# Kernel optimization log

Measured on AMD Instinct MI355X. Metric: run time of the kernel, lower is better.

Reference implementation:

```python
import jax, jax.numpy as jnp
import numpy as np

B, T, D_IN = 1024, 512, 32   # batch, sequence_length, input_dim
H = 512                      # hidden_dim
P = 96                       # prediction_length
D_OUT = 1                    # output_dim


def setup_inputs() -> dict:
    key = jax.random.key(0)
    ks = jax.random.split(key, 24)
    s = 1.0 / np.sqrt(H)  # PyTorch GRU default init scale
    u = lambda k, shape: jax.random.uniform(k, shape, jnp.float32, -s, s)
    inp = {"x": jax.random.normal(ks[0], (B, T, D_IN), jnp.float32)}
    # Encoder GRU: layer0 input D_IN, layer1 input H. Gate order: r, z, n.
    inp["enc_Wih0"] = u(ks[1], (3 * H, D_IN)); inp["enc_Whh0"] = u(ks[2], (3 * H, H))
    inp["enc_bih0"] = u(ks[3], (3 * H,));      inp["enc_bhh0"] = u(ks[4], (3 * H,))
    inp["enc_Wih1"] = u(ks[5], (3 * H, H));    inp["enc_Whh1"] = u(ks[6], (3 * H, H))
    inp["enc_bih1"] = u(ks[7], (3 * H,));      inp["enc_bhh1"] = u(ks[8], (3 * H,))
    # Decoder GRU: layer0 input D_OUT, layer1 input H.
    inp["dec_Wih0"] = u(ks[9], (3 * H, D_OUT)); inp["dec_Whh0"] = u(ks[10], (3 * H, H))
    inp["dec_bih0"] = u(ks[11], (3 * H,));      inp["dec_bhh0"] = u(ks[12], (3 * H,))
    inp["dec_Wih1"] = u(ks[13], (3 * H, H));    inp["dec_Whh1"] = u(ks[14], (3 * H, H))
    inp["dec_bih1"] = u(ks[15], (3 * H,));      inp["dec_bhh1"] = u(ks[16], (3 * H,))
    # Output projection + learned decoder start token.
    inp["out_W"] = u(ks[17], (D_OUT, H)); inp["out_b"] = u(ks[18], (D_OUT,))
    inp["dec_start"] = jnp.zeros((1, 1, D_OUT), jnp.float32)
    return inp


def gru_cell(x, h, Wih, Whh, bih, bhh):
    # PyTorch GRU cell: r,z,n gate order.
    gi = x @ Wih.T + bih          # [B, 3H]
    gh = h @ Whh.T + bhh          # [B, 3H]
    ir, iz, inn = jnp.split(gi, 3, axis=-1)
    hr, hz, hn = jnp.split(gh, 3, axis=-1)
    r = jax.nn.sigmoid(ir + hr)
    z = jax.nn.sigmoid(iz + hz)
    n = jnp.tanh(inn + r * hn)
    return (1.0 - z) * n + z * h


def reference(x,
              enc_Wih0, enc_Whh0, enc_bih0, enc_bhh0,
              enc_Wih1, enc_Whh1, enc_bih1, enc_bhh1,
              dec_Wih0, dec_Whh0, dec_bih0, dec_bhh0,
              dec_Wih1, dec_Whh1, dec_bih1, dec_bhh1,
              out_W, out_b, dec_start):
    Bsz = x.shape[0]
    h0 = jnp.zeros((Bsz, H), x.dtype)

    def enc_step(carry, xt):
        h1, h2 = carry
        h1 = gru_cell(xt, h1, enc_Wih0, enc_Whh0, enc_bih0, enc_bhh0)
        h2 = gru_cell(h1, h2, enc_Wih1, enc_Whh1, enc_bih1, enc_bhh1)
        return (h1, h2), None

    (h1, h2), _ = jax.lax.scan(enc_step, (h0, h0), jnp.swapaxes(x, 0, 1))

    y0 = jnp.broadcast_to(dec_start[0], (Bsz, D_OUT)).astype(x.dtype)

    def dec_step(carry, _):
        d1, d2, y = carry
        d1 = gru_cell(y, d1, dec_Wih0, dec_Whh0, dec_bih0, dec_bhh0)
        d2 = gru_cell(d1, d2, dec_Wih1, dec_Whh1, dec_bih1, dec_bhh1)
        y = d2 @ out_W.T + out_b  # [B, D_OUT]
        return (d1, d2, y), y

    _, ys = jax.lax.scan(dec_step, (h1, h2, y0), None, length=P)
    return jnp.swapaxes(ys, 0, 1)  # [B, P, D_OUT]
```

## Files before the change

kernel.cpp:

```cpp
#include <hip/hip_runtime.h>

#define HD 512
#define BB 1024
#define TT 512
#define PP 96
#define DIN 32
#define KC_H 16
#define NBLK 256
#define GRPB 16

typedef unsigned short u16;
typedef __attribute__((ext_vector_type(8))) short bf16x8;
typedef __attribute__((ext_vector_type(4))) float f32x4;
typedef __attribute__((address_space(3))) unsigned int lds_u32;
typedef __attribute__((address_space(3))) u16 lds_u16;
typedef __attribute__((address_space(1))) unsigned int glb_u32;

#define WAIT_VM(N) asm volatile("s_waitcnt vmcnt(" #N ")" ::: "memory")
__device__ __forceinline__ void bar_raw() { asm volatile("s_barrier" ::: "memory"); }

__device__ __forceinline__ float bf2f(u16 s) {
  return __uint_as_float(((unsigned)s) << 16);
}
__device__ __forceinline__ u16 f2bf_rne(float f) {
  unsigned u = __float_as_uint(f);
  u += 0x7FFF + ((u >> 16) & 1);
  return (u16)(u >> 16);
}
__device__ __forceinline__ float sigm(float v) { return 1.f / (1.f + __expf(-v)); }
__device__ __forceinline__ float tanh_(float a) {
  return 1.f - 2.f / (__expf(2.f * a) + 1.f);
}

__device__ __forceinline__ bf16x8 load_sc16(const u16* p) {
  bf16x8 r;
  asm volatile("global_load_dwordx4 %0, %1, off sc0 sc1" : "=&v"(r) : "v"(p) : "memory");
  return r;
}
__device__ __forceinline__ void store_sc_u16(u16* p, unsigned v) {
  asm volatile("global_store_short %0, %1, off sc0 sc1" :: "v"(p), "v"(v) : "memory");
}
__device__ __forceinline__ void store_sc_f32(float* p, float v) {
  asm volatile("global_store_dword %0, %1, off sc0 sc1" :: "v"(p), "v"(v) : "memory");
}
__device__ __forceinline__ float load_sc_f32w(const float* p) {
  float v;
  asm volatile("global_load_dword %0, %1, off sc0 sc1\ns_waitcnt vmcnt(0)"
               : "=&v"(v) : "v"(p) : "memory");
  return v;
}
__device__ __forceinline__ unsigned load_sc_u32w(const unsigned* p) {
  unsigned v;
  asm volatile("global_load_dword %0, %1, off sc0 sc1\ns_waitcnt vmcnt(0)"
               : "=&v"(v) : "v"(p) : "memory");
  return v;
}
__device__ __forceinline__ void store_h_sc(u16* H, u16* L, size_t idx, float hv) {
  u16 hi = (u16)(__float_as_uint(hv) >> 16);
  u16 lo = f2bf_rne(hv - bf2f(hi));
  store_sc_u16(H + idx, (unsigned)hi);
  store_sc_u16(L + idx, (unsigned)lo);
}

__global__ void pack_w_kernel(const float* __restrict__ W, int K,
                              u16* __restrict__ out) {
  int tid = blockIdx.x * 256 + threadIdx.x;
  int KC = K >> 5;
  int total = 16 * KC * 2 * 6 * 64;
  if (tid >= total) return;
  int lane = tid & 63;
  int rest = tid >> 6;
  int gs = rest % 6; rest /= 6;
  int fc = rest & 1; rest >>= 1;
  int kc = rest % KC;
  int jb = rest / KC;
  int g = gs >> 1, s = gs & 1;
  int j = jb * 32 + fc * 16 + (lane & 15);
  int k = kc * 32 + (lane >> 4) * 8;
  const float* src = W + (size_t)(g * HD + j) * K + k;
  bf16x8 v;
#pragma unroll
  for (int i = 0; i < 8; ++i) {
    float f = src[i];
    u16 hi = f2bf_rne(f);
    v[i] = (short)((s == 0) ? hi : f2bf_rne(f - bf2f(hi)));
  }
  *(bf16x8*)(out + (size_t)tid * 8) = v;
}

struct AF { bf16x8 h[2]; bf16x8 l[2]; };

__device__ __forceinline__ void fence_af(AF& a) {
  asm volatile("" : "+v"(a.h[0]), "+v"(a.h[1]), "+v"(a.l[0]), "+v"(a.l[1]));
}
__device__ __forceinline__ void load_af_sc(AF& a, const u16* aH0, const u16* aL0, int kc) {
  const u16* p = aH0 + kc * 32;
  const u16* q = aL0 + kc * 32;
  a.h[0] = load_sc16(p);
  a.h[1] = load_sc16(p + 16 * HD);
  a.l[0] = load_sc16(q);
  a.l[1] = load_sc16(q + 16 * HD);
}

__device__ __forceinline__ void mfma_kc_l(const lds_u16* base, int lane,
                                          const AF& a, f32x4* aR, f32x4* aZ, f32x4* aN) {
  typedef __attribute__((address_space(3))) const bf16x8 lds_bf16x8;
  const lds_u16* p = base + lane * 8;
#pragma unroll
  for (int g = 0; g < 3; ++g) {
    f32x4* acc = (g == 0) ? aR : (g == 1) ? aZ : aN;
    bf16x8 whi = *(lds_bf16x8*)(p + (g * 2 + 0) * 512);
    bf16x8 wlo = *(lds_bf16x8*)(p + (g * 2 + 1) * 512);
#pragma unroll
    for (int s = 0; s < 2; ++s) {
      acc[s] = __builtin_amdgcn_mfma_f32_16x16x32_bf16(a.h[s], whi, acc[s], 0, 0, 0);
      acc[s] = __builtin_amdgcn_mfma_f32_16x16x32_bf16(a.l[s], whi, acc[s], 0, 0, 0);
      acc[s] = __builtin_amdgcn_mfma_f32_16x16x32_bf16(a.h[s], wlo, acc[s], 0, 0, 0);
    }
  }
}
__device__ __forceinline__ void mfma_kc_g(const u16* base, int lane,
                                          const AF& a, f32x4* aR, f32x4* aZ, f32x4* aN) {
  const u16* p = base + lane * 8;
#pragma unroll
  for (int g = 0; g < 3; ++g) {
    f32x4* acc = (g == 0) ? aR : (g == 1) ? aZ : aN;
    bf16x8 whi = *(const bf16x8*)(p + (g * 2 + 0) * 512);
    bf16x8 wlo = *(const bf16x8*)(p + (g * 2 + 1) * 512);
#pragma unroll
    for (int s = 0; s < 2; ++s) {
      acc[s] = __builtin_amdgcn_mfma_f32_16x16x32_bf16(a.h[s], whi, acc[s], 0, 0, 0);
      acc[s] = __builtin_amdgcn_mfma_f32_16x16x32_bf16(a.l[s], whi, acc[s], 0, 0, 0);
      acc[s] = __builtin_amdgcn_mfma_f32_16x16x32_bf16(a.h[s], wlo, acc[s], 0, 0, 0);
    }
  }
}

__device__ __forceinline__ void stage6(const u16* src, u16* dst, int lane) {
#pragma unroll
  for (int j = 0; j < 6; ++j)
    __builtin_amdgcn_global_load_lds((const glb_u32*)(src + j * 512 + lane * 8),
                                     (lds_u32*)(dst + j * 512), 16, 0, 0);
}

template <bool DUAL>
__device__ __forceinline__ void pipe_phase(
    u16* ringfc, const u16* Ahi, const u16* Alo,
    const u16* WA, const u16* WB, int row0w, int lane, bool stg,
    f32x4* aR, f32x4* aZ, f32x4* aN,
    f32x4* bR, f32x4* bZ, f32x4* bN) {
  const int quad = lane >> 4, n16 = lane & 15;
  const u16* aH0 = Ahi + (size_t)(row0w + n16) * HD + quad * 8;
  const u16* aL0 = Alo + (size_t)(row0w + n16) * HD + quad * 8;
  u16* pb[4] = {ringfc, ringfc + 6144, ringfc + 2 * 6144, ringfc + 3 * 6144};
  AF a0, a1, a2, a3;

  auto issueB = [&](int ikc, u16* pair, AF& dst) {
    if (stg) {
      stage6(WA + (size_t)ikc * 6144, pair, lane);
      if constexpr (DUAL) stage6(WB + (size_t)ikc * 6144, pair + 3072, lane);
    }
    load_af_sc(dst, aH0, aL0, ikc);
  };
  auto cons = [&](u16* pair, AF& a) {
    fence_af(a);
    mfma_kc_l((const lds_u16*)pair, lane, a, aR, aZ, aN);
    if constexpr (DUAL) mfma_kc_l((const lds_u16*)(pair + 3072), lane, a, bR, bZ, bN);
  };
  auto wsteady = [&]() {
    if (stg) { if constexpr (DUAL) WAIT_VM(32); else WAIT_VM(20); }
    else WAIT_VM(8);
  };
  auto wtail1 = [&]() {
    if (stg) { if constexpr (DUAL) WAIT_VM(16); else WAIT_VM(10); }
    else WAIT_VM(4);
  };

  WAIT_VM(0);
  issueB(0, pb[0], a0);
  issueB(1, pb[1], a1);
  issueB(2, pb[2], a2);
#pragma unroll 1
  for (int kc = 0; kc < 12; kc += 4) {
    wsteady(); bar_raw(); issueB(kc + 3, pb[3], a3); cons(pb[0], a0);
    wsteady(); bar_raw(); issueB(kc + 4, pb[0], a0); cons(pb[1], a1);
    wsteady(); bar_raw(); issueB(kc + 5, pb[1], a1); cons(pb[2], a2);
    wsteady(); bar_raw(); issueB(kc + 6, pb[2], a2); cons(pb[3], a3);
  }
  wsteady(); bar_raw(); issueB(15, pb[3], a3); cons(pb[0], a0);
  wsteady(); bar_raw(); cons(pb[1], a1);
  wtail1();  bar_raw(); cons(pb[2], a2);
  WAIT_VM(0); bar_raw(); cons(pb[3], a3);
}

__device__ __forceinline__ void x_phase(const float* x, int t, const u16* Wp,
                                        int jb, int fc, int row0w, int lane,
                                        f32x4* aR, f32x4* aZ, f32x4* aN) {
  const int quad = lane >> 4, n16 = lane & 15;
  AF ax;
#pragma unroll
  for (int s = 0; s < 2; ++s) {
    const float* xp = x + (size_t)(row0w + s * 16 + n16) * (TT * DIN) +
                      (size_t)t * DIN + quad * 8;
    f32x4 v0 = *(const f32x4*)xp;
    f32x4 v1 = *(const f32x4*)(xp + 4);
    bf16x8 hi, lo;
#pragma unroll
    for (int i = 0; i < 8; ++i) {
      float f = (i < 4) ? v0[i] : v1[i - 4];
      u16 h = (u16)(__float_as_uint(f) >> 16);
      hi[i] = (short)h;
      lo[i] = (short)f2bf_rne(f - bf2f(h));
    }
    ax.h[s] = hi;
    ax.l[s] = lo;
  }
  mfma_kc_g(Wp + ((size_t)jb * 2 + fc) * 3072, lane, ax, aR, aZ, aN);
}

__device__ __forceinline__ void gbar(unsigned* gen, unsigned target) {
  WAIT_VM(0);
  __syncthreads();
  if (threadIdx.x == 0) {
    atomicAdd(gen, 1u);
    while (load_sc_u32w(gen) < target) __builtin_amdgcn_s_sleep(2);
  }
  __syncthreads();
}

__device__ __forceinline__ void gru_epi_reg(
    const float* bi, const float* bh, float (*ht)[4],
    u16* hnH, u16* hnL, int col, int row0w, int quad,
    const f32x4* aR, const f32x4* aZ, const f32x4* aNX, const f32x4* aNH) {
  const float bir = bi[col],          bhr = bh[col];
  const float biz = bi[HD + col],     bhz = bh[HD + col];
  const float bin = bi[2 * HD + col], bhn = bh[2 * HD + col];
#pragma unroll
  for (int s = 0; s < 2; ++s)
#pragma unroll
    for (int r = 0; r < 4; ++r) {
      const int row = row0w + s * 16 + quad * 4 + r;
      const size_t idx = (size_t)row * HD + col;
      float rr = sigm(aR[s][r] + bir + bhr);
      float zz = sigm(aZ[s][r] + biz + bhz);
      float nn = tanh_(aNX[s][r] + bin + rr * (aNH[s][r] + bhn));
      float hv = (1.f - zz) * nn + zz * ht[s][r];
      ht[s][r] = hv;
      store_h_sc(hnH, hnL, idx, hv);
    }
}

__global__ __launch_bounds__(256, 1)
void gru_persistent_kernel(
    const float* x,
    const u16* pkX0, const u16* pkH0, const float* bi0, const float* bh0,
    const u16* pkX1, const u16* pkH1, const float* bi1, const float* bh1,
    const u16* pkD0H, const float* dbi0, const float* dbh0, const float* dW0,
    const u16* pkD1I, const u16* pkD1H, const float* dbi1, const float* dbh1,
    const float* outW, const float* outb, const float* dstart,
    u16* h1aH, u16* h1aL, u16* h1bH, u16* h1bL,
    u16* h2aH, u16* h2aL, u16* h2bH, u16* h2bL,
    float* yfull, float* dout, unsigned* gen) {
  __shared__ u16 ring[2][4][6144];
  const int b = blockIdx.x;
  const int jb = (b & 7) * 2 + ((b >> 3) & 1);
  const int row0 = (b >> 4) * 64;
  const int tid = threadIdx.x, wave = tid >> 6, lane = tid & 63;
  const int quad = lane >> 4, n16 = lane & 15;
  const int fc = wave & 1, rowg = wave >> 1;
  const bool stg = (rowg == 0);
  const int row0w = row0 + rowg * 32;
  const int col = jb * 32 + fc * 16 + n16;
  u16* ringfc = &ring[fc][0][0];
  const f32x4 z4 = {0.f, 0.f, 0.f, 0.f};
  const size_t woff = ((size_t)jb * KC_H * 2 + fc) * 3072;
  unsigned* geng = gen + ((b >> 4) << 6);

  u16 *h1cH = h1aH, *h1cL = h1aL, *h1nH = h1bH, *h1nL = h1bL;
  u16 *h2cH = h2aH, *h2cL = h2aL, *h2nH = h2bH, *h2nL = h2bL;
  float ht1[2][4] = {{0, 0, 0, 0}, {0, 0, 0, 0}};
  float ht2[2][4] = {{0, 0, 0, 0}, {0, 0, 0, 0}};
  unsigned it = 0;

  for (int k = 0; k <= TT; ++k) {
    f32x4 R0[2] = {z4, z4}, Z0[2] = {z4, z4}, NX0[2] = {z4, z4}, NH0[2] = {z4, z4};
    f32x4 R1[2] = {z4, z4}, Z1[2] = {z4, z4}, NX1[2] = {z4, z4}, NH1[2] = {z4, z4};
    if (k > 0 && k < TT) {
      pipe_phase<true>(ringfc, h1cH, h1cL, pkH0 + woff, pkX1 + woff,
                       row0w, lane, stg, R0, Z0, NH0, R1, Z1, NX1);
    } else if (k == 0) {
      pipe_phase<false>(ringfc, h1cH, h1cL, pkH0 + woff, pkH0 + woff,
                        row0w, lane, stg, R0, Z0, NH0, R1, Z1, NX1);
    } else {
      pipe_phase<false>(ringfc, h1cH, h1cL, pkX1 + woff, pkX1 + woff,
                        row0w, lane, stg, R1, Z1, NX1, R0, Z0, NH0);
    }
    if (k < TT) {
      x_phase(x, k, pkX0, jb, fc, row0w, lane, R0, Z0, NX0);
      gru_epi_reg(bi0, bh0, ht1, h1nH, h1nL, col, row0w, quad, R0, Z0, NX0, NH0);
    }
    if (k > 0) {
      pipe_phase<false>(ringfc, h2cH, h2cL, pkH1 + woff, pkH1 + woff,
                        row0w, lane, stg, R1, Z1, NH1, R0, Z0, NX0);
      gru_epi_reg(bi1, bh1, ht2, h2nH, h2nL, col, row0w, quad, R1, Z1, NX1, NH1);
    }
    gbar(geng, GRPB * (++it));
    if (k < TT) { u16* t0 = h1cH; h1cH = h1nH; h1nH = t0;
                  u16* t1 = h1cL; h1cL = h1nL; h1nL = t1; }
    if (k > 0)  { u16* t0 = h2cH; h2cH = h2nH; h2nH = t0;
                  u16* t1 = h2cL; h2cL = h2nL; h2nL = t1; }
  }

  for (int t = 0; t < PP; ++t) {
    {
      f32x4 R[2] = {z4, z4}, Z[2] = {z4, z4}, NH[2] = {z4, z4};
      f32x4 D0[2] = {z4, z4}, D1[2] = {z4, z4}, D2[2] = {z4, z4};
      pipe_phase<false>(ringfc, h1cH, h1cL, pkD0H + woff, pkD0H + woff,
                        row0w, lane, stg, R, Z, NH, D0, D1, D2);
      float yl[2][4] = {{0, 0, 0, 0}, {0, 0, 0, 0}};
      if (t > 0) {
        const float* yb = yfull + ((t - 1) & 1) * BB;
#pragma unroll
        for (int s = 0; s < 2; ++s)
#pragma unroll
          for (int r = 0; r < 4; ++r) {
            const float* p = yb + (row0w + s * 16 + quad * 4 + r);
            asm volatile("global_load_dword %0, %1, off sc0 sc1"
                         : "=&v"(yl[s][r]) : "v"(p) : "memory");
          }
        WAIT_VM(0);
#pragma unroll
        for (int s = 0; s < 2; ++s)
#pragma unroll
          for (int r = 0; r < 4; ++r)
            asm volatile("" : "+v"(yl[s][r]));
      }
      const float ds0 = dstart[0], ob0 = outb[0];
      const float bir = dbi0[col],          bhr = dbh0[col];
      const float biz = dbi0[HD + col],     bhz = dbh0[HD + col];
      const float bin = dbi0[2 * HD + col], bhn = dbh0[2 * HD + col];
      const float w0r = dW0[col], w0z = dW0[HD + col], w0n = dW0[2 * HD + col];
#pragma unroll
      for (int s = 0; s < 2; ++s)
#pragma unroll
        for (int r = 0; r < 4; ++r) {
          const int row = row0w + s * 16 + quad * 4 + r;
          const size_t idx = (size_t)row * HD + col;
          float yv = (t == 0) ? ds0 : (ob0 + yl[s][r]);
          if (t > 0 && jb == 0 && fc == 0 && n16 == 0)
            dout[(size_t)row * PP + (t - 1)] = yv;
          float rr = sigm(R[s][r] + bir + bhr + yv * w0r);
          float zz = sigm(Z[s][r] + biz + bhz + yv * w0z);
          float nn = tanh_(bin + yv * w0n + rr * (NH[s][r] + bhn));
          float hv = (1.f - zz) * nn + zz * ht1[s][r];
          ht1[s][r] = hv;
          store_h_sc(h1nH, h1nL, idx, hv);
        }
    }
    gbar(geng, GRPB * (++it));
    {
      f32x4 R[2] = {z4, z4}, Z[2] = {z4, z4}, NX[2] = {z4, z4}, NH[2] = {z4, z4};
      f32x4 D0[2] = {z4, z4}, D1[2] = {z4, z4}, D2[2] = {z4, z4};
      pipe_phase<false>(ringfc, h1nH, h1nL, pkD1I + woff, pkD1I + woff,
                        row0w, lane, stg, R, Z, NX, D0, D1, D2);
      pipe_phase<false>(ringfc, h2cH, h2cL, pkD1H + woff, pkD1H + woff,
                        row0w, lane, stg, R, Z, NH, D0, D1, D2);
      const float bir = dbi1[col],          bhr = dbh1[col];
      const float biz = dbi1[HD + col],     bhz = dbh1[HD + col];
      const float bin = dbi1[2 * HD + col], bhn = dbh1[2 * HD + col];
      const float wo = outW[col];
      float* yw = yfull + (t & 1) * BB;
      float* yz = yfull + ((t - 1) & 1) * BB;
#pragma unroll
      for (int s = 0; s < 2; ++s)
#pragma unroll
        for (int r = 0; r < 4; ++r) {
          const int row = row0w + s * 16 + quad * 4 + r;
          const size_t idx = (size_t)row * HD + col;
          float rr = sigm(R[s][r] + bir + bhr);
          float zz = sigm(Z[s][r] + biz + bhz);
          float nn = tanh_(NX[s][r] + bin + rr * (NH[s][r] + bhn));
          float hv = (1.f - zz) * nn + zz * ht2[s][r];
          ht2[s][r] = hv;
          store_h_sc(h2nH, h2nL, idx, hv);
          float v = hv * wo;
#pragma unroll
          for (int off = 1; off < 16; off <<= 1) v += __shfl_xor(v, off, 16);
          if (n16 == 0) {
            atomicAdd(yw + row, v);
            if (t > 0 && jb == 0 && fc == 0) store_sc_f32(yz + row, 0.f);
          }
        }
    }
    gbar(geng, GRPB * (++it));
    { u16* t0 = h1cH; h1cH = h1nH; h1nH = t0;
      u16* t1 = h1cL; h1cL = h1nL; h1nL = t1; }
    { u16* t0 = h2cH; h2cH = h2nH; h2nH = t0;
      u16* t1 = h2cL; h2cL = h2nL; h2nL = t1; }
  }

  if ((b & 15) == 0 && tid < 64) {
    int row = row0 + tid;
    float v = load_sc_f32w(yfull + ((PP - 1) & 1) * BB + row);
    dout[(size_t)row * PP + (PP - 1)] = outb[0] + v;
  }
}

extern "C" void kernel_launch(void* const* d_in, const int* in_sizes, int n_in,
                              void* d_out, int out_size, void* d_ws, size_t ws_size,
                              hipStream_t stream) {
  const float* x      = (const float*)d_in[0];
  const float* eW_ih0 = (const float*)d_in[1];
  const float* eW_hh0 = (const float*)d_in[2];
  const float* eb_ih0 = (const float*)d_in[3];
  const float* eb_hh0 = (const float*)d_in[4];
  const float* eW_ih1 = (const float*)d_in[5];
  const float* eW_hh1 = (const float*)d_in[6];
  const float* eb_ih1 = (const float*)d_in[7];
  const float* eb_hh1 = (const float*)d_in[8];
  const float* dW_ih0 = (const float*)d_in[9];
  const float* dW_hh0 = (const float*)d_in[10];
  const float* db_ih0 = (const float*)d_in[11];
  const float* db_hh0 = (const float*)d_in[12];
  const float* dW_ih1 = (const float*)d_in[13];
  const float* dW_hh1 = (const float*)d_in[14];
  const float* db_ih1 = (const float*)d_in[15];
  const float* db_hh1 = (const float*)d_in[16];
  const float* outW   = (const float*)d_in[17];
  const float* outb   = (const float*)d_in[18];
  const float* dstart = (const float*)d_in[19];
  float* out = (float*)d_out;

  char* w = (char*)d_ws;
  size_t off = 0;
  auto carve = [&](size_t bytes) -> void* {
    void* p = w + off;
    off = (off + bytes + 255) & ~(size_t)255;
    return p;
  };
  u16* h1aH = (u16*)carve((size_t)BB * HD * 2); u16* h1aL = (u16*)carve((size_t)BB * HD * 2);
  u16* h1bH = (u16*)carve((size_t)BB * HD * 2); u16* h1bL = (u16*)carve((size_t)BB * HD * 2);
  u16* h2aH = (u16*)carve((size_t)BB * HD * 2); u16* h2aL = (u16*)carve((size_t)BB * HD * 2);
  u16* h2bH = (u16*)carve((size_t)BB * HD * 2); u16* h2bL = (u16*)carve((size_t)BB * HD * 2);
  float* yfull = (float*)carve((size_t)2 * BB * 4);
  unsigned* gen = (unsigned*)carve(4096);
  auto carve_pack = [&](int K) -> u16* {
    return (u16*)carve((size_t)3 * HD * K * 2 * 2);
  };
  u16* pk_e0ih = carve_pack(DIN);
  u16* pk_e0hh = carve_pack(HD);
  u16* pk_e1ih = carve_pack(HD);
  u16* pk_e1hh = carve_pack(HD);
  u16* pk_d0hh = carve_pack(HD);
  u16* pk_d1ih = carve_pack(HD);
  u16* pk_d1hh = carve_pack(HD);

  hipMemsetAsync(h1aH, 0, (size_t)BB * HD * 2, stream);
  hipMemsetAsync(h1aL, 0, (size_t)BB * HD * 2, stream);
  hipMemsetAsync(h2aH, 0, (size_t)BB * HD * 2, stream);
  hipMemsetAsync(h2aL, 0, (size_t)BB * HD * 2, stream);
  hipMemsetAsync(yfull, 0, (size_t)2 * BB * 4, stream);
  hipMemsetAsync(gen, 0, 4096, stream);

  auto pack = [&](const float* W, int K, u16* dst) {
    int total = 16 * (K >> 5) * 2 * 6 * 64;
    pack_w_kernel<<<(total + 255) / 256, 256, 0, stream>>>(W, K, dst);
  };
  pack(eW_ih0, DIN, pk_e0ih);
  pack(eW_hh0, HD, pk_e0hh);
  pack(eW_ih1, HD, pk_e1ih);
  pack(eW_hh1, HD, pk_e1hh);
  pack(dW_hh0, HD, pk_d0hh);
  pack(dW_ih1, HD, pk_d1ih);
  pack(dW_hh1, HD, pk_d1hh);

  gru_persistent_kernel<<<NBLK, 256, 0, stream>>>(
      x, pk_e0ih, pk_e0hh, eb_ih0, eb_hh0,
      pk_e1ih, pk_e1hh, eb_ih1, eb_hh1,
      pk_d0hh, db_ih0, db_hh0, dW_ih0,
      pk_d1ih, pk_d1hh, db_ih1, db_hh1,
      outW, outb, dstart,
      h1aH, h1aL, h1bH, h1bL, h2aH, h2aL, h2bH, h2bL,
      yfull, out, gen);
}
```

Measured before the change: 17.02 ms.

## Double waves per block, each wave handling 16 rows instead of 32

Each block now launches 512 threads instead of 256. Every wave computes one 16-row MFMA tile instead of two, which halves per-wave accumulator and A-fragment registers and doubles the number of waves per block. The vmcnt wait thresholds are reduced to match the smaller number of loads per stage. The aim is more latency hiding across waves, at the cost of more waves contending for the shared LDS ring and the barriers. launch_bounds is changed to (512, 2).

```diff
diff --git a/kernel.cpp b/kernel.cpp
--- a/kernel.cpp
+++ b/kernel.cpp
@@ -88,51 +88,41 @@
   *(bf16x8*)(out + (size_t)tid * 8) = v;
 }
 
-struct AF { bf16x8 h[2]; bf16x8 l[2]; };
+struct AF { bf16x8 h; bf16x8 l; };
 
 __device__ __forceinline__ void fence_af(AF& a) {
-  asm volatile("" : "+v"(a.h[0]), "+v"(a.h[1]), "+v"(a.l[0]), "+v"(a.l[1]));
+  asm volatile("" : "+v"(a.h), "+v"(a.l));
 }
 __device__ __forceinline__ void load_af_sc(AF& a, const u16* aH0, const u16* aL0, int kc) {
-  const u16* p = aH0 + kc * 32;
-  const u16* q = aL0 + kc * 32;
-  a.h[0] = load_sc16(p);
-  a.h[1] = load_sc16(p + 16 * HD);
-  a.l[0] = load_sc16(q);
-  a.l[1] = load_sc16(q + 16 * HD);
-}
-
-__device__ __forceinline__ void mfma_kc_l(const lds_u16* base, int lane,
-                                          const AF& a, f32x4* aR, f32x4* aZ, f32x4* aN) {
+  a.h = load_sc16(aH0 + kc * 32);
+  a.l = load_sc16(aL0 + kc * 32);
+}
+
+__device__ __forceinline__ void mfma_kc_l(const lds_u16* base, int lane, const AF& a,
+                                          f32x4& aR, f32x4& aZ, f32x4& aN) {
   typedef __attribute__((address_space(3))) const bf16x8 lds_bf16x8;
   const lds_u16* p = base + lane * 8;
 #pragma unroll
   for (int g = 0; g < 3; ++g) {
-    f32x4* acc = (g == 0) ? aR : (g == 1) ? aZ : aN;
+    f32x4* acc = (g == 0) ? &aR : (g == 1) ? &aZ : &aN;
     bf16x8 whi = *(lds_bf16x8*)(p + (g * 2 + 0) * 512);
     bf16x8 wlo = *(lds_bf16x8*)(p + (g * 2 + 1) * 512);
-#pragma unroll
-    for (int s = 0; s < 2; ++s) {
-      acc[s] = __builtin_amdgcn_mfma_f32_16x16x32_bf16(a.h[s], whi, acc[s], 0, 0, 0);
-      acc[s] = __builtin_amdgcn_mfma_f32_16x16x32_bf16(a.l[s], whi, acc[s], 0, 0, 0);
-      acc[s] = __builtin_amdgcn_mfma_f32_16x16x32_bf16(a.h[s], wlo, acc[s], 0, 0, 0);
-    }
-  }
-}
-__device__ __forceinline__ void mfma_kc_g(const u16* base, int lane,
-                                          const AF& a, f32x4* aR, f32x4* aZ, f32x4* aN) {
+    *acc = __builtin_amdgcn_mfma_f32_16x16x32_bf16(a.h, whi, *acc, 0, 0, 0);
+    *acc = __builtin_amdgcn_mfma_f32_16x16x32_bf16(a.l, whi, *acc, 0, 0, 0);
+    *acc = __builtin_amdgcn_mfma_f32_16x16x32_bf16(a.h, wlo, *acc, 0, 0, 0);
+  }
+}
+__device__ __forceinline__ void mfma_kc_g(const u16* base, int lane, const AF& a,
+                                          f32x4& aR, f32x4& aZ, f32x4& aN) {
   const u16* p = base + lane * 8;
 #pragma unroll
   for (int g = 0; g < 3; ++g) {
-    f32x4* acc = (g == 0) ? aR : (g == 1) ? aZ : aN;
+    f32x4* acc = (g == 0) ? &aR : (g == 1) ? &aZ : &aN;
     bf16x8 whi = *(const bf16x8*)(p + (g * 2 + 0) * 512);
     bf16x8 wlo = *(const bf16x8*)(p + (g * 2 + 1) * 512);
-#pragma unroll
-    for (int s = 0; s < 2; ++s) {
-      acc[s] = __builtin_amdgcn_mfma_f32_16x16x32_bf16(a.h[s], whi, acc[s], 0, 0, 0);
-      acc[s] = __builtin_amdgcn_mfma_f32_16x16x32_bf16(a.l[s], whi, acc[s], 0, 0, 0);
-      acc[s] = __builtin_amdgcn_mfma_f32_16x16x32_bf16(a.h[s], wlo, acc[s], 0, 0, 0);
-    }
+    *acc = __builtin_amdgcn_mfma_f32_16x16x32_bf16(a.h, whi, *acc, 0, 0, 0);
+    *acc = __builtin_amdgcn_mfma_f32_16x16x32_bf16(a.l, whi, *acc, 0, 0, 0);
+    *acc = __builtin_amdgcn_mfma_f32_16x16x32_bf16(a.h, wlo, *acc, 0, 0, 0);
   }
 }
 
@@ -147,8 +137,8 @@
 __device__ __forceinline__ void pipe_phase(
     u16* ringfc, const u16* Ahi, const u16* Alo,
     const u16* WA, const u16* WB, int row0w, int lane, bool stg,
-    f32x4* aR, f32x4* aZ, f32x4* aN,
-    f32x4* bR, f32x4* bZ, f32x4* bN) {
+    f32x4& aR, f32x4& aZ, f32x4& aN,
+    f32x4& bR, f32x4& bZ, f32x4& bN) {
   const int quad = lane >> 4, n16 = lane & 15;
   const u16* aH0 = Ahi + (size_t)(row0w + n16) * HD + quad * 8;
   const u16* aL0 = Alo + (size_t)(row0w + n16) * HD + quad * 8;
@@ -168,12 +158,12 @@
     if constexpr (DUAL) mfma_kc_l((const lds_u16*)(pair + 3072), lane, a, bR, bZ, bN);
   };
   auto wsteady = [&]() {
-    if (stg) { if constexpr (DUAL) WAIT_VM(32); else WAIT_VM(20); }
-    else WAIT_VM(8);
+    if (stg) { if constexpr (DUAL) WAIT_VM(28); else WAIT_VM(16); }
+    else WAIT_VM(4);
   };
   auto wtail1 = [&]() {
-    if (stg) { if constexpr (DUAL) WAIT_VM(16); else WAIT_VM(10); }
-    else WAIT_VM(4);
+    if (stg) { if constexpr (DUAL) WAIT_VM(14); else WAIT_VM(8); }
+    else WAIT_VM(2);
   };
 
   WAIT_VM(0);
@@ -195,26 +185,23 @@
 
 __device__ __forceinline__ void x_phase(const float* x, int t, const u16* Wp,
                                         int jb, int fc, int row0w, int lane,
-                                        f32x4* aR, f32x4* aZ, f32x4* aN) {
+                                        f32x4& aR, f32x4& aZ, f32x4& aN) {
   const int quad = lane >> 4, n16 = lane & 15;
   AF ax;
-#pragma unroll
-  for (int s = 0; s < 2; ++s) {
-    const float* xp = x + (size_t)(row0w + s * 16 + n16) * (TT * DIN) +
-                      (size_t)t * DIN + quad * 8;
-    f32x4 v0 = *(const f32x4*)xp;
-    f32x4 v1 = *(const f32x4*)(xp + 4);
-    bf16x8 hi, lo;
-#pragma unroll
-    for (int i = 0; i < 8; ++i) {
-      float f = (i < 4) ? v0[i] : v1[i - 4];
-      u16 h = (u16)(__float_as_uint(f) >> 16);
-      hi[i] = (short)h;
-      lo[i] = (short)f2bf_rne(f - bf2f(h));
-    }
-    ax.h[s] = hi;
-    ax.l[s] = lo;
-  }
+  const float* xp = x + (size_t)(row0w + n16) * (TT * DIN) +
+                    (size_t)t * DIN + quad * 8;
+  f32x4 v0 = *(const f32x4*)xp;
+  f32x4 v1 = *(const f32x4*)(xp + 4);
+  bf16x8 hi, lo;
+#pragma unroll
+  for (int i = 0; i < 8; ++i) {
+    float f = (i < 4) ? v0[i] : v1[i - 4];
+    u16 h = (u16)(__float_as_uint(f) >> 16);
+    hi[i] = (short)h;
+    lo[i] = (short)f2bf_rne(f - bf2f(h));
+  }
+  ax.h = hi;
+  ax.l = lo;
   mfma_kc_g(Wp + ((size_t)jb * 2 + fc) * 3072, lane, ax, aR, aZ, aN);
 }
 
@@ -229,28 +216,26 @@
 }
 
 __device__ __forceinline__ void gru_epi_reg(
-    const float* bi, const float* bh, float (*ht)[4],
+    const float* bi, const float* bh, float* ht,
     u16* hnH, u16* hnL, int col, int row0w, int quad,
-    const f32x4* aR, const f32x4* aZ, const f32x4* aNX, const f32x4* aNH) {
+    const f32x4& aR, const f32x4& aZ, const f32x4& aNX, const f32x4& aNH) {
   const float bir = bi[col],          bhr = bh[col];
   const float biz = bi[HD + col],     bhz = bh[HD + col];
   const float bin = bi[2 * HD + col], bhn = bh[2 * HD + col];
 #pragma unroll
-  for (int s = 0; s < 2; ++s)
-#pragma unroll
-    for (int r = 0; r < 4; ++r) {
-      const int row = row0w + s * 16 + quad * 4 + r;
-      const size_t idx = (size_t)row * HD + col;
-      float rr = sigm(aR[s][r] + bir + bhr);
-      float zz = sigm(aZ[s][r] + biz + bhz);
-      float nn = tanh_(aNX[s][r] + bin + rr * (aNH[s][r] + bhn));
-      float hv = (1.f - zz) * nn + zz * ht[s][r];
-      ht[s][r] = hv;
-      store_h_sc(hnH, hnL, idx, hv);
-    }
-}
-
-__global__ __launch_bounds__(256, 1)
+  for (int r = 0; r < 4; ++r) {
+    const int row = row0w + quad * 4 + r;
+    const size_t idx = (size_t)row * HD + col;
+    float rr = sigm(aR[r] + bir + bhr);
+    float zz = sigm(aZ[r] + biz + bhz);
+    float nn = tanh_(aNX[r] + bin + rr * (aNH[r] + bhn));
+    float hv = (1.f - zz) * nn + zz * ht[r];
+    ht[r] = hv;
+    store_h_sc(hnH, hnL, idx, hv);
+  }
+}
+
+__global__ __launch_bounds__(512, 2)
 void gru_persistent_kernel(
     const float* x,
     const u16* pkX0, const u16* pkH0, const float* bi0, const float* bh0,
@@ -269,7 +254,7 @@
   const int quad = lane >> 4, n16 = lane & 15;
   const int fc = wave & 1, rowg = wave >> 1;
   const bool stg = (rowg == 0);
-  const int row0w = row0 + rowg * 32;
+  const int row0w = row0 + rowg * 16;
   const int col = jb * 32 + fc * 16 + n16;
   u16* ringfc = &ring[fc][0][0];
   const f32x4 z4 = {0.f, 0.f, 0.f, 0.f};
@@ -278,13 +263,13 @@
 
   u16 *h1cH = h1aH, *h1cL = h1aL, *h1nH = h1bH, *h1nL = h1bL;
   u16 *h2cH = h2aH, *h2cL = h2aL, *h2nH = h2bH, *h2nL = h2bL;
-  float ht1[2][4] = {{0, 0, 0, 0}, {0, 0, 0, 0}};
-  float ht2[2][4] = {{0, 0, 0, 0}, {0, 0, 0, 0}};
+  float ht1[4] = {0, 0, 0, 0};
+  float ht2[4] = {0, 0, 0, 0};
   unsigned it = 0;
 
   for (int k = 0; k <= TT; ++k) {
-    f32x4 R0[2] = {z4, z4}, Z0[2] = {z4, z4}, NX0[2] = {z4, z4}, NH0[2] = {z4, z4};
-    f32x4 R1[2] = {z4, z4}, Z1[2] = {z4, z4}, NX1[2] = {z4, z4}, NH1[2] = {z4, z4};
+    f32x4 R0 = z4, Z0 = z4, NX0 = z4, NH0 = z4;
+    f32x4 R1 = z4, Z1 = z4, NX1 = z4, NH1 = z4;
     if (k > 0 && k < TT) {
       pipe_phase<true>(ringfc, h1cH, h1cL, pkH0 + woff, pkX1 + woff,
                        row0w, lane, stg, R0, Z0, NH0, R1, Z1, NX1);
@@ -313,27 +298,23 @@
 
   for (int t = 0; t < PP; ++t) {
     {
-      f32x4 R[2] = {z4, z4}, Z[2] = {z4, z4}, NH[2] = {z4, z4};
-      f32x4 D0[2] = {z4, z4}, D1[2] = {z4, z4}, D2[2] = {z4, z4};
+      f32x4 R = z4, Z = z4, NH = z4;
+      f32x4 D0 = z4, D1 = z4, D2 = z4;
       pipe_phase<false>(ringfc, h1cH, h1cL, pkD0H + woff, pkD0H + woff,
                         row0w, lane, stg, R, Z, NH, D0, D1, D2);
-      float yl[2][4] = {{0, 0, 0, 0}, {0, 0, 0, 0}};
+      float yl[4] = {0, 0, 0, 0};
       if (t > 0) {
         const float* yb = yfull + ((t - 1) & 1) * BB;
 #pragma unroll
-        for (int s = 0; s < 2; ++s)
-#pragma unroll
-          for (int r = 0; r < 4; ++r) {
-            const float* p = yb + (row0w + s * 16 + quad * 4 + r);
-            asm volatile("global_load_dword %0, %1, off sc0 sc1"
-                         : "=&v"(yl[s][r]) : "v"(p) : "memory");
-          }
+        for (int r = 0; r < 4; ++r) {
+          const float* p = yb + (row0w + quad * 4 + r);
+          asm volatile("global_load_dword %0, %1, off sc0 sc1"
+                       : "=&v"(yl[r]) : "v"(p) : "memory");
+        }
         WAIT_VM(0);
 #pragma unroll
-        for (int s = 0; s < 2; ++s)
-#pragma unroll
-          for (int r = 0; r < 4; ++r)
-            asm volatile("" : "+v"(yl[s][r]));
+        for (int r = 0; r < 4; ++r)
+          asm volatile("" : "+v"(yl[r]));
       }
       const float ds0 = dstart[0], ob0 = outb[0];
       const float bir = dbi0[col],          bhr = dbh0[col];
@@ -341,26 +322,24 @@
       const float bin = dbi0[2 * HD + col], bhn = dbh0[2 * HD + col];
       const float w0r = dW0[col], w0z = dW0[HD + col], w0n = dW0[2 * HD + col];
 #pragma unroll
-      for (int s = 0; s < 2; ++s)
-#pragma unroll
-        for (int r = 0; r < 4; ++r) {
-          const int row = row0w + s * 16 + quad * 4 + r;
-          const size_t idx = (size_t)row * HD + col;
-          float yv = (t == 0) ? ds0 : (ob0 + yl[s][r]);
-          if (t > 0 && jb == 0 && fc == 0 && n16 == 0)
-            dout[(size_t)row * PP + (t - 1)] = yv;
-          float rr = sigm(R[s][r] + bir + bhr + yv * w0r);
-          float zz = sigm(Z[s][r] + biz + bhz + yv * w0z);
-          float nn = tanh_(bin + yv * w0n + rr * (NH[s][r] + bhn));
-          float hv = (1.f - zz) * nn + zz * ht1[s][r];
-          ht1[s][r] = hv;
-          store_h_sc(h1nH, h1nL, idx, hv);
-        }
+      for (int r = 0; r < 4; ++r) {
+        const int row = row0w + quad * 4 + r;
+        const size_t idx = (size_t)row * HD + col;
+        float yv = (t == 0) ? ds0 : (ob0 + yl[r]);
+        if (t > 0 && jb == 0 && fc == 0 && n16 == 0)
+          dout[(size_t)row * PP + (t - 1)] = yv;
+        float rr = sigm(R[r] + bir + bhr + yv * w0r);
+        float zz = sigm(Z[r] + biz + bhz + yv * w0z);
+        float nn = tanh_(bin + yv * w0n + rr * (NH[r] + bhn));
+        float hv = (1.f - zz) * nn + zz * ht1[r];
+        ht1[r] = hv;
+        store_h_sc(h1nH, h1nL, idx, hv);
+      }
     }
     gbar(geng, GRPB * (++it));
     {
-      f32x4 R[2] = {z4, z4}, Z[2] = {z4, z4}, NX[2] = {z4, z4}, NH[2] = {z4, z4};
-      f32x4 D0[2] = {z4, z4}, D1[2] = {z4, z4}, D2[2] = {z4, z4};
+      f32x4 R = z4, Z = z4, NX = z4, NH = z4;
+      f32x4 D0 = z4, D1 = z4, D2 = z4;
       pipe_phase<false>(ringfc, h1nH, h1nL, pkD1I + woff, pkD1I + woff,
                         row0w, lane, stg, R, Z, NX, D0, D1, D2);
       pipe_phase<false>(ringfc, h2cH, h2cL, pkD1H + woff, pkD1H + woff,
@@ -372,25 +351,23 @@
       float* yw = yfull + (t & 1) * BB;
       float* yz = yfull + ((t - 1) & 1) * BB;
 #pragma unroll
-      for (int s = 0; s < 2; ++s)
-#pragma unroll
-        for (int r = 0; r < 4; ++r) {
-          const int row = row0w + s * 16 + quad * 4 + r;
-          const size_t idx = (size_t)row * HD + col;
-          float rr = sigm(R[s][r] + bir + bhr);
-          float zz = sigm(Z[s][r] + biz + bhz);
-          float nn = tanh_(NX[s][r] + bin + rr * (NH[s][r] + bhn));
-          float hv = (1.f - zz) * nn + zz * ht2[s][r];
-          ht2[s][r] = hv;
-          store_h_sc(h2nH, h2nL, idx, hv);
-          float v = hv * wo;
-#pragma unroll
-          for (int off = 1; off < 16; off <<= 1) v += __shfl_xor(v, off, 16);
-          if (n16 == 0) {
-            atomicAdd(yw + row, v);
-            if (t > 0 && jb == 0 && fc == 0) store_sc_f32(yz + row, 0.f);
-          }
+      for (int r = 0; r < 4; ++r) {
+        const int row = row0w + quad * 4 + r;
+        const size_t idx = (size_t)row * HD + col;
+        float rr = sigm(R[r] + bir + bhr);
+        float zz = sigm(Z[r] + biz + bhz);
+        float nn = tanh_(NX[r] + bin + rr * (NH[r] + bhn));
+        float hv = (1.f - zz) * nn + zz * ht2[r];
+        ht2[r] = hv;
+        store_h_sc(h2nH, h2nL, idx, hv);
+        float v = hv * wo;
+#pragma unroll
+        for (int off = 1; off < 16; off <<= 1) v += __shfl_xor(v, off, 16);
+        if (n16 == 0) {
+          atomicAdd(yw + row, v);
+          if (t > 0 && jb == 0 && fc == 0) store_sc_f32(yz + row, 0.f);
         }
+      }
     }
     gbar(geng, GRPB * (++it));
     { u16* t0 = h1cH; h1cH = h1nH; h1nH = t0;
@@ -474,7 +451,7 @@
   pack(dW_ih1, HD, pk_d1ih);
   pack(dW_hh1, HD, pk_d1hh);
 
-  gru_persistent_kernel<<<NBLK, 256, 0, stream>>>(
+  gru_persistent_kernel<<<NBLK, 512, 0, stream>>>(
       x, pk_e0ih, pk_e0hh, eb_ih0, eb_hh0,
       pk_e1ih, pk_e1hh, eb_ih1, eb_hh1,
       pk_d0hh, db_ih0, db_hh0, dW_ih0,
```

After: 20.29 ms. 1.19x slower.
